# Kernel tuning notes

Hardware: AMD Instinct MI355X
Metric: run time of the kernel (lower is better)

Reference implementation:

```python
import jax, jax.numpy as jnp
import numpy as np

B, H, L, D = 4, 16, 2048, 64
NEG = -1.0e9


def setup_inputs() -> dict:
    key = jax.random.key(0)
    kq, kk, kv, km = jax.random.split(key, 4)
    q = jax.random.normal(kq, (B, H, L, D), dtype=jnp.float32)
    k = jax.random.normal(kk, (B, H, L, D), dtype=jnp.float32)
    v = jax.random.normal(kv, (B, H, L, D), dtype=jnp.float32)
    # padding mask: 1.0 = masked position, 0.0 = keep (broadcast over heads and query positions)
    mask = jax.random.randint(km, (B, 1, 1, L), 0, 2).astype(jnp.float32)
    return {"q": q, "k": k, "v": v, "mask": mask}


def reference(q, k, v, mask):
    # scores: [B,H,Lq,Lk]
    dk = jnp.asarray(q.shape[-1], dtype=q.dtype)
    logits = jnp.einsum("bhqd,bhkd->bhqk", q, k) / jnp.sqrt(dk)
    logits = logits + mask * NEG
    attn = jax.nn.softmax(logits, axis=-1)
    out = jnp.einsum("bhqk,bhkd->bhqd", attn, v)
    return out, attn
```

## Files before the change

### kernel.cpp

```cpp
#include <hip/hip_runtime.h>


#define LL 2048
#define DD 64
#define HH 16
#define TQ 64
#define TK 64
#define NTH 256
#define NKT (LL / TK)

typedef __attribute__((ext_vector_type(8))) short bf16x8;
typedef __attribute__((ext_vector_type(4))) float f32x4;

__device__ __forceinline__ unsigned short bf_hi(float x) {
    return (unsigned short)(__float_as_uint(x) >> 16);
}
__device__ __forceinline__ float bf_f(unsigned short h) {
    return __uint_as_float(((unsigned int)h) << 16);
}
__device__ __forceinline__ int swz(int row, int col) {
    return (row << 6) + (col ^ ((row & 7) << 3));
}

__global__ __launch_bounds__(NTH, 3)
void attn_mfma(const float* __restrict__ Q, const float* __restrict__ K,
               const float* __restrict__ V, const float* __restrict__ M,
               float* __restrict__ Out, float* __restrict__ Attn)
{
    __shared__ __align__(16) unsigned short s_kh[TK * DD];
    __shared__ __align__(16) unsigned short s_kl[TK * DD];
    __shared__ __align__(16) unsigned short s_vh[DD * TK];
    __shared__ __align__(16) unsigned short s_vl[DD * TK];
    __shared__ __align__(16) unsigned int   s_p [TQ * TK];

    const int tid  = threadIdx.x;
    const int wid  = tid >> 6;
    const int lane = tid & 63;
    const int lg   = lane >> 4;
    const int ln   = lane & 15;

    const int bh  = blockIdx.y;
    const int b   = bh >> 4;
    const int q0b = blockIdx.x * TQ;
    const size_t rowBH = (size_t)bh * LL;

    const int sr = tid >> 2;
    const int sc = (tid & 3) << 4;
    const int vd  = tid & 63;
    const int vk0 = (tid >> 6) << 2;

    const float* Mrow = M + b * LL;
    const f32x4 fzero = {0.f, 0.f, 0.f, 0.f};

    {
        const float* qp = Q + (rowBH + q0b + sr) * DD;
        #pragma unroll
        for (int i = 0; i < 4; ++i) {
            float4 x = *(const float4*)(qp + sc + (i << 2));
            ushort4 h, l;
            h.x = bf_hi(x.x); l.x = bf_hi(x.x - bf_f(h.x));
            h.y = bf_hi(x.y); l.y = bf_hi(x.y - bf_f(h.y));
            h.z = bf_hi(x.z); l.z = bf_hi(x.z - bf_f(h.z));
            h.w = bf_hi(x.w); l.w = bf_hi(x.w - bf_f(h.w));
            int a = swz(sr, sc + (i << 2));
            *(ushort4*)&s_kh[a] = h;
            *(ushort4*)&s_kl[a] = l;
        }
    }
    __syncthreads();

    bf16x8 qh[2], ql[2];
    {
        const int qrow = (wid << 4) + ln;
        #pragma unroll
        for (int s = 0; s < 2; ++s) {
            int a = swz(qrow, (s << 5) + (lg << 3));
            qh[s] = *(const bf16x8*)&s_kh[a];
            ql[s] = *(const bf16x8*)&s_kl[a];
        }
    }
    __syncthreads();

    float esum[4] = {0.f, 0.f, 0.f, 0.f};

    for (int kt = 0; kt < NKT; ++kt) {
        {
            const float* kp = K + (rowBH + kt * TK + sr) * DD;
            #pragma unroll
            for (int i = 0; i < 4; ++i) {
                float4 x = *(const float4*)(kp + sc + (i << 2));
                ushort4 h;
                h.x = bf_hi(x.x); h.y = bf_hi(x.y);
                h.z = bf_hi(x.z); h.w = bf_hi(x.w);
                *(ushort4*)&s_kh[swz(sr, sc + (i << 2))] = h;
            }
        }
        __syncthreads();

        f32x4 acc[4];
        #pragma unroll
        for (int ct = 0; ct < 4; ++ct) acc[ct] = fzero;

        #pragma unroll
        for (int s = 0; s < 2; ++s) {
            #pragma unroll
            for (int ct = 0; ct < 4; ++ct) {
                bf16x8 kh = *(const bf16x8*)&s_kh[swz((ct << 4) + ln, (s << 5) + (lg << 3))];
                acc[ct] = __builtin_amdgcn_mfma_f32_16x16x32_bf16(qh[s], kh, acc[ct], 0, 0, 0);
            }
        }

        #pragma unroll
        for (int ct = 0; ct < 4; ++ct) {
            float mneg = Mrow[kt * TK + (ct << 4) + ln] * -1.0e9f;
            #pragma unroll
            for (int r = 0; r < 4; ++r)
                esum[r] += __expf(fmaf(acc[ct][r], 0.125f, mneg));
        }
        __syncthreads();
    }

    #pragma unroll
    for (int m = 1; m <= 8; m <<= 1) {
        #pragma unroll
        for (int r = 0; r < 4; ++r)
            esum[r] += __shfl_xor(esum[r], m, 64);
    }
    float inv[4];
    #pragma unroll
    for (int r = 0; r < 4; ++r) inv[r] = 1.0f / esum[r];

    f32x4 oacc[4];
    #pragma unroll
    for (int dt = 0; dt < 4; ++dt) oacc[dt] = fzero;

    for (int kt = 0; kt < NKT; ++kt) {
        {
            const float* kp = K + (rowBH + kt * TK + sr) * DD;
            #pragma unroll
            for (int i = 0; i < 4; ++i) {
                float4 x = *(const float4*)(kp + sc + (i << 2));
                ushort4 h, l;
                h.x = bf_hi(x.x); l.x = bf_hi(x.x - bf_f(h.x));
                h.y = bf_hi(x.y); l.y = bf_hi(x.y - bf_f(h.y));
                h.z = bf_hi(x.z); l.z = bf_hi(x.z - bf_f(h.z));
                h.w = bf_hi(x.w); l.w = bf_hi(x.w - bf_f(h.w));
                int a = swz(sr, sc + (i << 2));
                *(ushort4*)&s_kh[a] = h;
                *(ushort4*)&s_kl[a] = l;
            }
            const float* vbase = V + (rowBH + kt * TK) * DD + vd;
            #pragma unroll
            for (int i = 0; i < 4; ++i) {
                int kb = vk0 + (i << 4);
                float x0 = vbase[(kb + 0) * DD];
                float x1 = vbase[(kb + 1) * DD];
                float x2 = vbase[(kb + 2) * DD];
                float x3 = vbase[(kb + 3) * DD];
                ushort4 h, l;
                h.x = bf_hi(x0); l.x = bf_hi(x0 - bf_f(h.x));
                h.y = bf_hi(x1); l.y = bf_hi(x1 - bf_f(h.y));
                h.z = bf_hi(x2); l.z = bf_hi(x2 - bf_f(h.z));
                h.w = bf_hi(x3); l.w = bf_hi(x3 - bf_f(h.w));
                int a = swz(vd, kb);
                *(ushort4*)&s_vh[a] = h;
                *(ushort4*)&s_vl[a] = l;
            }
        }
        __syncthreads();

        f32x4 acc[4];
        #pragma unroll
        for (int ct = 0; ct < 4; ++ct) acc[ct] = fzero;

        #pragma unroll
        for (int s = 0; s < 2; ++s) {
            #pragma unroll
            for (int ct = 0; ct < 4; ++ct) {
                int a = swz((ct << 4) + ln, (s << 5) + (lg << 3));
                bf16x8 kh = *(const bf16x8*)&s_kh[a];
                bf16x8 kl = *(const bf16x8*)&s_kl[a];
                acc[ct] = __builtin_amdgcn_mfma_f32_16x16x32_bf16(qh[s], kh, acc[ct], 0, 0, 0);
                acc[ct] = __builtin_amdgcn_mfma_f32_16x16x32_bf16(qh[s], kl, acc[ct], 0, 0, 0);
                acc[ct] = __builtin_amdgcn_mfma_f32_16x16x32_bf16(ql[s], kh, acc[ct], 0, 0, 0);
            }
        }

        float* ap = Attn + (rowBH + q0b + (wid << 4) + (lg << 2)) * (size_t)LL
                  + (size_t)kt * TK + ln;
        #pragma unroll
        for (int ct = 0; ct < 4; ++ct) {
            float mneg = Mrow[kt * TK + (ct << 4) + ln] * -1.0e9f;
            #pragma unroll
            for (int r = 0; r < 4; ++r) {
                float p = __expf(fmaf(acc[ct][r], 0.125f, mneg)) * inv[r];
                ap[(size_t)r * LL + (ct << 4)] = p;
                unsigned short php = bf_hi(p);
                unsigned short plp = bf_hi(p - bf_f(php));
                s_p[swz((wid << 4) + (lg << 2) + r, (ct << 4) + ln)] =
                    (unsigned int)php | ((unsigned int)plp << 16);
            }
        }

        #pragma unroll
        for (int s2 = 0; s2 < 2; ++s2) {
            int pa = swz((wid << 4) + ln, (s2 << 5) + (lg << 3));
            uint4 w0 = *(const uint4*)&s_p[pa];
            uint4 w1 = *(const uint4*)&s_p[pa + 4];
            unsigned int wv[8] = {w0.x, w0.y, w0.z, w0.w, w1.x, w1.y, w1.z, w1.w};
            bf16x8 pfh, pfl;
            #pragma unroll
            for (int e = 0; e < 8; ++e) {
                pfh[e] = (short)(wv[e] & 0xffffu);
                pfl[e] = (short)(wv[e] >> 16);
            }
            #pragma unroll
            for (int dt = 0; dt < 4; ++dt) {
                int a = swz((dt << 4) + ln, (s2 << 5) + (lg << 3));
                bf16x8 vh = *(const bf16x8*)&s_vh[a];
                bf16x8 vl = *(const bf16x8*)&s_vl[a];
                oacc[dt] = __builtin_amdgcn_mfma_f32_16x16x32_bf16(pfh, vh, oacc[dt], 0, 0, 0);
                oacc[dt] = __builtin_amdgcn_mfma_f32_16x16x32_bf16(pfh, vl, oacc[dt], 0, 0, 0);
                oacc[dt] = __builtin_amdgcn_mfma_f32_16x16x32_bf16(pfl, vh, oacc[dt], 0, 0, 0);
            }
        }
        __syncthreads();
    }

    float* op = Out + (rowBH + q0b + (wid << 4) + (lg << 2)) * DD + ln;
    #pragma unroll
    for (int dt = 0; dt < 4; ++dt)
        #pragma unroll
        for (int r = 0; r < 4; ++r)
            op[r * DD + (dt << 4)] = oacc[dt][r];
}

extern "C" void kernel_launch(void* const* d_in, const int* in_sizes, int n_in,
                              void* d_out, int out_size, void* d_ws, size_t ws_size,
                              hipStream_t stream) {
    const float* Q = (const float*)d_in[0];
    const float* K = (const float*)d_in[1];
    const float* V = (const float*)d_in[2];
    const float* M = (const float*)d_in[3];
    float* Out  = (float*)d_out;
    float* Attn = Out + (size_t)4 * HH * LL * DD;

    dim3 grid(LL / TQ, 4 * HH);
    dim3 block(NTH);
    attn_mfma<<<grid, block, 0, stream>>>(Q, K, V, M, Out, Attn);
}
```

Baseline: 1.506 ms.

## Double query tile per block, prefetch K/V into registers, remap block order

Each block now handles 128 query rows, with each wave owning two 16-row MFMA tiles. This reuses every staged K/V tile across twice as many queries and halves global K/V traffic and conversion work. Q is loaded straight into registers, and the next K/V tile is prefetched into registers while the current one is used. The change also adds s_setprio around the MFMA sections, a padded P buffer, and a swizzled block index for L2 locality. The grid dimensions in kernel_launch are not updated (still LL/TQ by 64), so the fid remap assumes a 16-wide grid. Occupancy falls to 2 blocks because of higher register use.

```diff
diff --git a/kernel.cpp b/kernel.cpp
--- a/kernel.cpp
+++ b/kernel.cpp
@@ -4,25 +4,26 @@
 #define LL 2048
 #define DD 64
 #define HH 16
-#define TQ 64
+#define TQ 128
 #define TK 64
 #define NTH 256
 #define NKT (LL / TK)
+#define SPD 66
 
 typedef __attribute__((ext_vector_type(8))) short bf16x8;
 typedef __attribute__((ext_vector_type(4))) float f32x4;
 
-__device__ __forceinline__ unsigned short bf_hi(float x) {
+static __device__ __forceinline__ unsigned short bf_hi(float x) {
     return (unsigned short)(__float_as_uint(x) >> 16);
 }
-__device__ __forceinline__ float bf_f(unsigned short h) {
+static __device__ __forceinline__ float bf_f(unsigned short h) {
     return __uint_as_float(((unsigned int)h) << 16);
 }
-__device__ __forceinline__ int swz(int row, int col) {
+static __device__ __forceinline__ int swz(int row, int col) {
     return (row << 6) + (col ^ ((row & 7) << 3));
 }
 
-__global__ __launch_bounds__(NTH, 3)
+__global__ __launch_bounds__(NTH, 2)
 void attn_mfma(const float* __restrict__ Q, const float* __restrict__ K,
                const float* __restrict__ V, const float* __restrict__ M,
                float* __restrict__ Out, float* __restrict__ Attn)
@@ -31,7 +32,7 @@
     __shared__ __align__(16) unsigned short s_kl[TK * DD];
     __shared__ __align__(16) unsigned short s_vh[DD * TK];
     __shared__ __align__(16) unsigned short s_vl[DD * TK];
-    __shared__ __align__(16) unsigned int   s_p [TQ * TK];
+    __shared__ __align__(16) unsigned int   s_p [TQ * SPD];
 
     const int tid  = threadIdx.x;
     const int wid  = tid >> 6;
@@ -39,140 +40,173 @@
     const int lg   = lane >> 4;
     const int ln   = lane & 15;
 
-    const int bh  = blockIdx.y;
-    const int b   = bh >> 4;
-    const int q0b = blockIdx.x * TQ;
+    int fid = blockIdx.y * 16 + blockIdx.x;
+    fid = (fid & 7) * 128 + (fid >> 3);
+    const int bx = fid & 15;
+    const int bh = fid >> 4;
+    const int b  = bh >> 4;
+    const int q0b = bx * TQ;
     const size_t rowBH = (size_t)bh * LL;
 
-    const int sr = tid >> 2;
-    const int sc = (tid & 3) << 4;
+    const int sr  = tid >> 2;
+    const int sc  = (tid & 3) << 4;
     const int vd  = tid & 63;
     const int vk0 = (tid >> 6) << 2;
 
     const float* Mrow = M + b * LL;
-    const f32x4 fzero = {0.f, 0.f, 0.f, 0.f};
-
+    const f32x4 fz = {0.f, 0.f, 0.f, 0.f};
+
+    bf16x8 qh[2][2], ql[2][2];
+    #pragma unroll
+    for (int rt = 0; rt < 2; ++rt) {
+        const float* qp = Q + (rowBH + q0b + (wid << 5) + (rt << 4) + ln) * DD;
+        #pragma unroll
+        for (int s = 0; s < 2; ++s) {
+            float4 x0 = *(const float4*)(qp + (s << 5) + (lg << 3));
+            float4 x1 = *(const float4*)(qp + (s << 5) + (lg << 3) + 4);
+            float f[8] = {x0.x, x0.y, x0.z, x0.w, x1.x, x1.y, x1.z, x1.w};
+            bf16x8 h, l;
+            #pragma unroll
+            for (int e = 0; e < 8; ++e) {
+                unsigned short hh = bf_hi(f[e]);
+                h[e] = (short)hh;
+                l[e] = (short)bf_hi(f[e] - bf_f(hh));
+            }
+            qh[rt][s] = h;
+            ql[rt][s] = l;
+        }
+    }
+
+    float esum[2][4] = {};
+    float4 kr[4];
     {
-        const float* qp = Q + (rowBH + q0b + sr) * DD;
+        const float* kp = K + (rowBH + sr) * DD + sc;
+        #pragma unroll
+        for (int i = 0; i < 4; ++i) kr[i] = *(const float4*)(kp + (i << 2));
+    }
+    for (int kt = 0; kt < NKT; ++kt) {
         #pragma unroll
         for (int i = 0; i < 4; ++i) {
-            float4 x = *(const float4*)(qp + sc + (i << 2));
+            ushort4 h;
+            h.x = bf_hi(kr[i].x); h.y = bf_hi(kr[i].y);
+            h.z = bf_hi(kr[i].z); h.w = bf_hi(kr[i].w);
+            *(ushort4*)&s_kh[swz(sr, sc + (i << 2))] = h;
+        }
+        __syncthreads();
+        if (kt + 1 < NKT) {
+            const float* kp = K + (rowBH + (kt + 1) * TK + sr) * DD + sc;
+            #pragma unroll
+            for (int i = 0; i < 4; ++i) kr[i] = *(const float4*)(kp + (i << 2));
+        }
+
+        f32x4 acc[2][4];
+        #pragma unroll
+        for (int rt = 0; rt < 2; ++rt)
+            #pragma unroll
+            for (int ct = 0; ct < 4; ++ct) acc[rt][ct] = fz;
+
+        __builtin_amdgcn_s_setprio(1);
+        #pragma unroll
+        for (int s = 0; s < 2; ++s) {
+            #pragma unroll
+            for (int ct = 0; ct < 4; ++ct) {
+                bf16x8 kh = *(const bf16x8*)&s_kh[swz((ct << 4) + ln, (s << 5) + (lg << 3))];
+                #pragma unroll
+                for (int rt = 0; rt < 2; ++rt)
+                    acc[rt][ct] = __builtin_amdgcn_mfma_f32_16x16x32_bf16(qh[rt][s], kh, acc[rt][ct], 0, 0, 0);
+            }
+        }
+        __builtin_amdgcn_s_setprio(0);
+
+        #pragma unroll
+        for (int ct = 0; ct < 4; ++ct) {
+            float mneg = Mrow[kt * TK + (ct << 4) + ln] * -1.0e9f;
+            #pragma unroll
+            for (int rt = 0; rt < 2; ++rt)
+                #pragma unroll
+                for (int r = 0; r < 4; ++r)
+                    esum[rt][r] += __expf(fmaf(acc[rt][ct][r], 0.125f, mneg));
+        }
+        __syncthreads();
+    }
+
+    #pragma unroll
+    for (int m = 1; m <= 8; m <<= 1)
+        #pragma unroll
+        for (int rt = 0; rt < 2; ++rt)
+            #pragma unroll
+            for (int r = 0; r < 4; ++r)
+                esum[rt][r] += __shfl_xor(esum[rt][r], m, 64);
+    float inv[2][4];
+    #pragma unroll
+    for (int rt = 0; rt < 2; ++rt)
+        #pragma unroll
+        for (int r = 0; r < 4; ++r) inv[rt][r] = 1.0f / esum[rt][r];
+
+    f32x4 oacc[2][4];
+    #pragma unroll
+    for (int rt = 0; rt < 2; ++rt)
+        #pragma unroll
+        for (int dt = 0; dt < 4; ++dt) oacc[rt][dt] = fz;
+
+    float4 kr2[4];
+    float  vr[16];
+    {
+        const float* kp = K + (rowBH + sr) * DD + sc;
+        #pragma unroll
+        for (int i = 0; i < 4; ++i) kr2[i] = *(const float4*)(kp + (i << 2));
+        const float* vbase = V + rowBH * DD + vd;
+        #pragma unroll
+        for (int i = 0; i < 4; ++i)
+            #pragma unroll
+            for (int j = 0; j < 4; ++j)
+                vr[(i << 2) + j] = vbase[(vk0 + (i << 4) + j) * DD];
+    }
+
+    for (int kt = 0; kt < NKT; ++kt) {
+        #pragma unroll
+        for (int i = 0; i < 4; ++i) {
             ushort4 h, l;
-            h.x = bf_hi(x.x); l.x = bf_hi(x.x - bf_f(h.x));
-            h.y = bf_hi(x.y); l.y = bf_hi(x.y - bf_f(h.y));
-            h.z = bf_hi(x.z); l.z = bf_hi(x.z - bf_f(h.z));
-            h.w = bf_hi(x.w); l.w = bf_hi(x.w - bf_f(h.w));
+            h.x = bf_hi(kr2[i].x); l.x = bf_hi(kr2[i].x - bf_f(h.x));
+            h.y = bf_hi(kr2[i].y); l.y = bf_hi(kr2[i].y - bf_f(h.y));
+            h.z = bf_hi(kr2[i].z); l.z = bf_hi(kr2[i].z - bf_f(h.z));
+            h.w = bf_hi(kr2[i].w); l.w = bf_hi(kr2[i].w - bf_f(h.w));
             int a = swz(sr, sc + (i << 2));
             *(ushort4*)&s_kh[a] = h;
             *(ushort4*)&s_kl[a] = l;
         }
-    }
-    __syncthreads();
-
-    bf16x8 qh[2], ql[2];
-    {
-        const int qrow = (wid << 4) + ln;
-        #pragma unroll
-        for (int s = 0; s < 2; ++s) {
-            int a = swz(qrow, (s << 5) + (lg << 3));
-            qh[s] = *(const bf16x8*)&s_kh[a];
-            ql[s] = *(const bf16x8*)&s_kl[a];
-        }
-    }
-    __syncthreads();
-
-    float esum[4] = {0.f, 0.f, 0.f, 0.f};
-
-    for (int kt = 0; kt < NKT; ++kt) {
-        {
-            const float* kp = K + (rowBH + kt * TK + sr) * DD;
-            #pragma unroll
-            for (int i = 0; i < 4; ++i) {
-                float4 x = *(const float4*)(kp + sc + (i << 2));
-                ushort4 h;
-                h.x = bf_hi(x.x); h.y = bf_hi(x.y);
-                h.z = bf_hi(x.z); h.w = bf_hi(x.w);
-                *(ushort4*)&s_kh[swz(sr, sc + (i << 2))] = h;
-            }
+        #pragma unroll
+        for (int i = 0; i < 4; ++i) {
+            ushort4 h, l;
+            h.x = bf_hi(vr[(i << 2) + 0]); l.x = bf_hi(vr[(i << 2) + 0] - bf_f(h.x));
+            h.y = bf_hi(vr[(i << 2) + 1]); l.y = bf_hi(vr[(i << 2) + 1] - bf_f(h.y));
+            h.z = bf_hi(vr[(i << 2) + 2]); l.z = bf_hi(vr[(i << 2) + 2] - bf_f(h.z));
+            h.w = bf_hi(vr[(i << 2) + 3]); l.w = bf_hi(vr[(i << 2) + 3] - bf_f(h.w));
+            int a = swz(vd, vk0 + (i << 4));
+            *(ushort4*)&s_vh[a] = h;
+            *(ushort4*)&s_vl[a] = l;
         }
         __syncthreads();
 
-        f32x4 acc[4];
-        #pragma unroll
-        for (int ct = 0; ct < 4; ++ct) acc[ct] = fzero;
-
-        #pragma unroll
-        for (int s = 0; s < 2; ++s) {
-            #pragma unroll
-            for (int ct = 0; ct < 4; ++ct) {
-                bf16x8 kh = *(const bf16x8*)&s_kh[swz((ct << 4) + ln, (s << 5) + (lg << 3))];
-                acc[ct] = __builtin_amdgcn_mfma_f32_16x16x32_bf16(qh[s], kh, acc[ct], 0, 0, 0);
-            }
-        }
-
-        #pragma unroll
-        for (int ct = 0; ct < 4; ++ct) {
-            float mneg = Mrow[kt * TK + (ct << 4) + ln] * -1.0e9f;
-            #pragma unroll
-            for (int r = 0; r < 4; ++r)
-                esum[r] += __expf(fmaf(acc[ct][r], 0.125f, mneg));
-        }
-        __syncthreads();
-    }
-
-    #pragma unroll
-    for (int m = 1; m <= 8; m <<= 1) {
-        #pragma unroll
-        for (int r = 0; r < 4; ++r)
-            esum[r] += __shfl_xor(esum[r], m, 64);
-    }
-    float inv[4];
-    #pragma unroll
-    for (int r = 0; r < 4; ++r) inv[r] = 1.0f / esum[r];
-
-    f32x4 oacc[4];
-    #pragma unroll
-    for (int dt = 0; dt < 4; ++dt) oacc[dt] = fzero;
-
-    for (int kt = 0; kt < NKT; ++kt) {
-        {
-            const float* kp = K + (rowBH + kt * TK + sr) * DD;
-            #pragma unroll
-            for (int i = 0; i < 4; ++i) {
-                float4 x = *(const float4*)(kp + sc + (i << 2));
-                ushort4 h, l;
-                h.x = bf_hi(x.x); l.x = bf_hi(x.x - bf_f(h.x));
-                h.y = bf_hi(x.y); l.y = bf_hi(x.y - bf_f(h.y));
-                h.z = bf_hi(x.z); l.z = bf_hi(x.z - bf_f(h.z));
-                h.w = bf_hi(x.w); l.w = bf_hi(x.w - bf_f(h.w));
-                int a = swz(sr, sc + (i << 2));
-                *(ushort4*)&s_kh[a] = h;
-                *(ushort4*)&s_kl[a] = l;
-            }
-            const float* vbase = V + (rowBH + kt * TK) * DD + vd;
-            #pragma unroll
-            for (int i = 0; i < 4; ++i) {
-                int kb = vk0 + (i << 4);
-                float x0 = vbase[(kb + 0) * DD];
-                float x1 = vbase[(kb + 1) * DD];
-                float x2 = vbase[(kb + 2) * DD];
-                float x3 = vbase[(kb + 3) * DD];
-                ushort4 h, l;
-                h.x = bf_hi(x0); l.x = bf_hi(x0 - bf_f(h.x));
-                h.y = bf_hi(x1); l.y = bf_hi(x1 - bf_f(h.y));
-                h.z = bf_hi(x2); l.z = bf_hi(x2 - bf_f(h.z));
-                h.w = bf_hi(x3); l.w = bf_hi(x3 - bf_f(h.w));
-                int a = swz(vd, kb);
-                *(ushort4*)&s_vh[a] = h;
-                *(ushort4*)&s_vl[a] = l;
-            }
-        }
-        __syncthreads();
-
-        f32x4 acc[4];
-        #pragma unroll
-        for (int ct = 0; ct < 4; ++ct) acc[ct] = fzero;
-
+        if (kt + 1 < NKT) {
+            const float* kp = K + (rowBH + (kt + 1) * TK + sr) * DD + sc;
+            #pragma unroll
+            for (int i = 0; i < 4; ++i) kr2[i] = *(const float4*)(kp + (i << 2));
+            const float* vbase = V + (rowBH + (kt + 1) * TK) * DD + vd;
+            #pragma unroll
+            for (int i = 0; i < 4; ++i)
+                #pragma unroll
+                for (int j = 0; j < 4; ++j)
+                    vr[(i << 2) + j] = vbase[(vk0 + (i << 4) + j) * DD];
+        }
+
+        f32x4 acc[2][4];
+        #pragma unroll
+        for (int rt = 0; rt < 2; ++rt)
+            #pragma unroll
+            for (int ct = 0; ct < 4; ++ct) acc[rt][ct] = fz;
+
+        __builtin_amdgcn_s_setprio(1);
         #pragma unroll
         for (int s = 0; s < 2; ++s) {
             #pragma unroll
@@ -180,59 +214,81 @@
                 int a = swz((ct << 4) + ln, (s << 5) + (lg << 3));
                 bf16x8 kh = *(const bf16x8*)&s_kh[a];
                 bf16x8 kl = *(const bf16x8*)&s_kl[a];
-                acc[ct] = __builtin_amdgcn_mfma_f32_16x16x32_bf16(qh[s], kh, acc[ct], 0, 0, 0);
-                acc[ct] = __builtin_amdgcn_mfma_f32_16x16x32_bf16(qh[s], kl, acc[ct], 0, 0, 0);
-                acc[ct] = __builtin_amdgcn_mfma_f32_16x16x32_bf16(ql[s], kh, acc[ct], 0, 0, 0);
-            }
-        }
-
-        float* ap = Attn + (rowBH + q0b + (wid << 4) + (lg << 2)) * (size_t)LL
-                  + (size_t)kt * TK + ln;
-        #pragma unroll
-        for (int ct = 0; ct < 4; ++ct) {
-            float mneg = Mrow[kt * TK + (ct << 4) + ln] * -1.0e9f;
-            #pragma unroll
-            for (int r = 0; r < 4; ++r) {
-                float p = __expf(fmaf(acc[ct][r], 0.125f, mneg)) * inv[r];
-                ap[(size_t)r * LL + (ct << 4)] = p;
-                unsigned short php = bf_hi(p);
-                unsigned short plp = bf_hi(p - bf_f(php));
-                s_p[swz((wid << 4) + (lg << 2) + r, (ct << 4) + ln)] =
-                    (unsigned int)php | ((unsigned int)plp << 16);
+                #pragma unroll
+                for (int rt = 0; rt < 2; ++rt) {
+                    acc[rt][ct] = __builtin_amdgcn_mfma_f32_16x16x32_bf16(qh[rt][s], kh, acc[rt][ct], 0, 0, 0);
+                    acc[rt][ct] = __builtin_amdgcn_mfma_f32_16x16x32_bf16(qh[rt][s], kl, acc[rt][ct], 0, 0, 0);
+                    acc[rt][ct] = __builtin_amdgcn_mfma_f32_16x16x32_bf16(ql[rt][s], kh, acc[rt][ct], 0, 0, 0);
+                }
+            }
+        }
+        __builtin_amdgcn_s_setprio(0);
+
+        #pragma unroll
+        for (int rt = 0; rt < 2; ++rt) {
+            const int prow = (wid << 5) + (rt << 4) + (lg << 2);
+            float* ap = Attn + (rowBH + q0b + prow) * (size_t)LL + (size_t)kt * TK + ln;
+            #pragma unroll
+            for (int ct = 0; ct < 4; ++ct) {
+                float mneg = Mrow[kt * TK + (ct << 4) + ln] * -1.0e9f;
+                #pragma unroll
+                for (int r = 0; r < 4; ++r) {
+                    float p = __expf(fmaf(acc[rt][ct][r], 0.125f, mneg)) * inv[rt][r];
+                    ap[(size_t)r * LL + (ct << 4)] = p;
+                    unsigned short hp = bf_hi(p);
+                    unsigned short lp = bf_hi(p - bf_f(hp));
+                    s_p[(prow + r) * SPD + (ct << 4) + ln] =
+                        (unsigned int)hp | ((unsigned int)lp << 16);
+                }
             }
         }
 
         #pragma unroll
         for (int s2 = 0; s2 < 2; ++s2) {
-            int pa = swz((wid << 4) + ln, (s2 << 5) + (lg << 3));
-            uint4 w0 = *(const uint4*)&s_p[pa];
-            uint4 w1 = *(const uint4*)&s_p[pa + 4];
-            unsigned int wv[8] = {w0.x, w0.y, w0.z, w0.w, w1.x, w1.y, w1.z, w1.w};
-            bf16x8 pfh, pfl;
-            #pragma unroll
-            for (int e = 0; e < 8; ++e) {
-                pfh[e] = (short)(wv[e] & 0xffffu);
-                pfl[e] = (short)(wv[e] >> 16);
-            }
+            bf16x8 pfh[2], pfl[2];
+            #pragma unroll
+            for (int rt = 0; rt < 2; ++rt) {
+                const unsigned int* pp =
+                    &s_p[((wid << 5) + (rt << 4) + ln) * SPD + (s2 << 5) + (lg << 3)];
+                uint4 w0 = *(const uint4*)pp;
+                uint4 w1 = *(const uint4*)(pp + 4);
+                unsigned int wv[8] = {w0.x, w0.y, w0.z, w0.w, w1.x, w1.y, w1.z, w1.w};
+                bf16x8 fh, fl;
+                #pragma unroll
+                for (int e = 0; e < 8; ++e) {
+                    fh[e] = (short)(wv[e] & 0xffffu);
+                    fl[e] = (short)(wv[e] >> 16);
+                }
+                pfh[rt] = fh;
+                pfl[rt] = fl;
+            }
+            __builtin_amdgcn_s_setprio(1);
             #pragma unroll
             for (int dt = 0; dt < 4; ++dt) {
                 int a = swz((dt << 4) + ln, (s2 << 5) + (lg << 3));
                 bf16x8 vh = *(const bf16x8*)&s_vh[a];
                 bf16x8 vl = *(const bf16x8*)&s_vl[a];
-                oacc[dt] = __builtin_amdgcn_mfma_f32_16x16x32_bf16(pfh, vh, oacc[dt], 0, 0, 0);
-                oacc[dt] = __builtin_amdgcn_mfma_f32_16x16x32_bf16(pfh, vl, oacc[dt], 0, 0, 0);
-                oacc[dt] = __builtin_amdgcn_mfma_f32_16x16x32_bf16(pfl, vh, oacc[dt], 0, 0, 0);
-            }
+                #pragma unroll
+                for (int rt = 0; rt < 2; ++rt) {
+                    oacc[rt][dt] = __builtin_amdgcn_mfma_f32_16x16x32_bf16(pfh[rt], vh, oacc[rt][dt], 0, 0, 0);
+                    oacc[rt][dt] = __builtin_amdgcn_mfma_f32_16x16x32_bf16(pfh[rt], vl, oacc[rt][dt], 0, 0, 0);
+                    oacc[rt][dt] = __builtin_amdgcn_mfma_f32_16x16x32_bf16(pfl[rt], vh, oacc[rt][dt], 0, 0, 0);
+                }
+            }
+            __builtin_amdgcn_s_setprio(0);
         }
         __syncthreads();
     }
 
-    float* op = Out + (rowBH + q0b + (wid << 4) + (lg << 2)) * DD + ln;
-    #pragma unroll
-    for (int dt = 0; dt < 4; ++dt)
-        #pragma unroll
-        for (int r = 0; r < 4; ++r)
-            op[r * DD + (dt << 4)] = oacc[dt][r];
+    #pragma unroll
+    for (int rt = 0; rt < 2; ++rt) {
+        float* op = Out + (rowBH + q0b + (wid << 5) + (rt << 4) + (lg << 2)) * DD + ln;
+        #pragma unroll
+        for (int dt = 0; dt < 4; ++dt)
+            #pragma unroll
+            for (int r = 0; r < 4; ++r)
+                op[r * DD + (dt << 4)] = oacc[rt][dt][r];
+    }
 }
 
 extern "C" void kernel_launch(void* const* d_in, const int* in_sizes, int n_in,
```

After: 1.413 ms. 6.2% less time.
